# Kernel optimization log

Measured on AMD Instinct MI355X. Metric: run time of the kernel, lower is better.

## Reference

```python
import jax, jax.numpy as jnp
import numpy as np

EPS = 1e-07
INF = 100000.0
BIG = 1e8  # sentinel cost for priors outside all gt boxes/centers (filtered out in torch)
CENTER_RADIUS = 2.5
CANDIDATE_TOPK = 10
IOU_WEIGHT = 3.0
CLS_WEIGHT = 1.0
IMG = 1280.0


def setup_inputs() -> dict:
    key = jax.random.key(0)
    ks = jax.random.split(key, 9)
    N, G, C = 33600, 128, 80
    cx = jax.random.uniform(ks[0], (N,), minval=0.0, maxval=IMG)
    cy = jax.random.uniform(ks[1], (N,), minval=0.0, maxval=IMG)
    strides = jax.random.uniform(ks[2], (N, 2), minval=8.0, maxval=32.0)
    priors = jnp.stack([cx, cy, strides[:, 0], strides[:, 1]], axis=1)  # [N,4] cx,cy,sw,sh
    dc = jax.random.uniform(ks[3], (N, 2), minval=0.0, maxval=IMG)
    dwh = jax.random.uniform(ks[4], (N, 2), minval=4.0, maxval=200.0)
    decoded_bboxes = jnp.concatenate([dc - dwh / 2, dc + dwh / 2], axis=1)  # [N,4] tlbr
    gc = jax.random.uniform(ks[5], (G, 2), minval=0.0, maxval=IMG)
    gwh = jax.random.uniform(ks[6], (G, 2), minval=20.0, maxval=400.0)
    gt_bboxes = jnp.concatenate([gc - gwh / 2, gc + gwh / 2], axis=1)  # [G,4] tlbr
    pred_scores = jax.random.uniform(ks[7], (N, C), minval=1e-4, maxval=1.0 - 1e-4)
    gt_labels = jax.random.randint(ks[8], (G,), 0, C)
    return {
        'pred_scores': pred_scores,
        'priors': priors,
        'decoded_bboxes': decoded_bboxes,
        'gt_bboxes': gt_bboxes,
        'gt_labels': gt_labels,
    }


def _pairwise_iou(a, b):
    # a: [N,4] tlbr, b: [G,4] tlbr -> [N,G]
    tl = jnp.maximum(a[:, None, :2], b[None, :, :2])
    br = jnp.minimum(a[:, None, 2:], b[None, :, 2:])
    wh = jnp.clip(br - tl, 0.0)
    inter = wh[..., 0] * wh[..., 1]
    area_a = jnp.prod(jnp.clip(a[:, 2:] - a[:, :2], 0.0), axis=-1)
    area_b = jnp.prod(jnp.clip(b[:, 2:] - b[:, :2], 0.0), axis=-1)
    union = area_a[:, None] + area_b[None, :] - inter
    return inter / jnp.maximum(union, EPS)


def _forward(pred_scores, priors, decoded_bboxes, gt_bboxes, gt_labels):
    N = decoded_bboxes.shape[0]
    G = gt_bboxes.shape[0]
    px, py = priors[:, 0:1], priors[:, 1:2]          # [N,1]
    sx, sy = priors[:, 2:3], priors[:, 3:4]
    # in-gt-box mask [N,G]
    l_ = px - gt_bboxes[None, :, 0]
    t_ = py - gt_bboxes[None, :, 1]
    r_ = gt_bboxes[None, :, 2] - px
    b_ = gt_bboxes[None, :, 3] - py
    is_in_gts = jnp.minimum(jnp.minimum(l_, t_), jnp.minimum(r_, b_)) > 0
    # in-center mask [N,G]
    gcx = (gt_bboxes[:, 0] + gt_bboxes[:, 2]) / 2.0
    gcy = (gt_bboxes[:, 1] + gt_bboxes[:, 3]) / 2.0
    cl_ = px - (gcx[None, :] - CENTER_RADIUS * sx)
    ct_ = py - (gcy[None, :] - CENTER_RADIUS * sy)
    cr_ = (gcx[None, :] + CENTER_RADIUS * sx) - px
    cb_ = (gcy[None, :] + CENTER_RADIUS * sy) - py
    is_in_cts = jnp.minimum(jnp.minimum(cl_, ct_), jnp.minimum(cr_, cb_)) > 0
    valid = jnp.any(is_in_gts | is_in_cts, axis=1)           # [N]
    in_box_and_center = is_in_gts & is_in_cts                # [N,G]

    ious = _pairwise_iou(decoded_bboxes, gt_bboxes)          # [N,G]
    ious = jnp.where(valid[:, None], ious, 0.0)              # invalid priors excluded
    iou_cost = -jnp.log(ious + EPS)

    # BCE(pred, one_hot(label)).sum(-1) without materializing [N,G,C]:
    # = -log p[label] + log1p(-p[label]) - sum_c log1p(-p_c)  (logs clamped at -100 like torch)
    L = jnp.clip(jnp.log(pred_scores), -100.0)               # [N,C]
    L1 = jnp.clip(jnp.log1p(-pred_scores), -100.0)           # [N,C]
    gl = gt_labels.astype(jnp.int32)
    cls_cost = -(L[:, gl] - L1[:, gl]) - jnp.sum(L1, axis=1, keepdims=True)  # [N,G]

    cost = cls_cost * CLS_WEIGHT + iou_cost * IOU_WEIGHT + (~in_box_and_center) * INF
    cost = jnp.where(valid[:, None], cost, BIG)

    K = min(CANDIDATE_TOPK, N)
    topk_ious, _ = jax.lax.top_k(ious.T, K)                  # [G,K]
    dynamic_ks = jnp.clip(topk_ious.sum(1).astype(jnp.int32), 1, None)  # [G], <= K
    # per-GT: K smallest costs (ascending), keep first dynamic_k of them
    _, pos_idx = jax.lax.top_k(-cost.T, K)                   # [G,K] prior indices
    sel = (jnp.arange(K)[None, :] < dynamic_ks[:, None]).astype(cost.dtype)
    matching = jnp.zeros((N, G), cost.dtype).at[pos_idx, jnp.arange(G)[:, None]].add(sel)

    # resolve priors matched to >1 gt by min-cost gt
    multi = matching.sum(1) > 1
    argmin = jnp.argmin(cost, axis=1)
    matching = jnp.where(multi[:, None], jax.nn.one_hot(argmin, G, dtype=cost.dtype), matching)

    fg = matching.sum(1) > 0
    matched_gt = jnp.argmax(matching, axis=1)
    matched_iou = jnp.sum(matching * ious, axis=1)

    assigned_gt_inds = jnp.where(fg, matched_gt, 0)
    assigned_labels = jnp.where(fg, 1, -1)
    assigned_gt_iou = jnp.where(fg, matched_iou, -INF)
    return assigned_gt_inds, assigned_labels, assigned_gt_iou


def reference(pred_scores, priors, decoded_bboxes, gt_bboxes, gt_labels):
    return _forward(pred_scores, priors, decoded_bboxes, gt_bboxes, gt_labels)
```

## Files before the change

kernel.cpp:

```cpp
#include <hip/hip_runtime.h>
#include <math.h>
#include <limits.h>

#pragma clang fp contract(off)

#define TPB 256
#define ATPB 64
#define KTOP 10
#define ISPLIT 64
#define GSPLIT 8
#define GCAP 4096
#define CHUNKCAP 4224
#define MAXG 512
#define MAXMULTI 4096

typedef unsigned int u32;
typedef unsigned long long u64;
typedef unsigned char u8;

__device__ __forceinline__ float f_iou(float ax0, float ay0, float ax1, float ay1,
                                       float bx0, float by0, float bx1, float by1) {
  float tlx = fmaxf(ax0, bx0);
  float tly = fmaxf(ay0, by0);
  float brx = fminf(ax1, bx1);
  float bry = fminf(ay1, by1);
  float w = fmaxf(brx - tlx, 0.0f);
  float h = fmaxf(bry - tly, 0.0f);
  float inter = w * h;
  float aa = fmaxf(ax1 - ax0, 0.0f) * fmaxf(ay1 - ay0, 0.0f);
  float ab = fmaxf(bx1 - bx0, 0.0f) * fmaxf(by1 - by0, 0.0f);
  float uni = aa + ab - inter;
  return inter / fmaxf(uni, 1e-7f);
}

__device__ __forceinline__ float f_dv(float p) {
  float L  = fmaxf(logf(p), -100.0f);
  float L1 = fmaxf(log1pf(-p), -100.0f);
  return -(L - L1);
}

__device__ __forceinline__ float f_cost(float iou_masked, float dv, float sumL1v,
                                        float px, float py, float sx, float sy,
                                        float bx0, float by0, float bx1, float by1,
                                        int vld) {
  if (!vld) return 100000000.0f;
  float cls = dv - sumL1v;
  float l_ = px - bx0, t_ = py - by0, r_ = bx1 - px, b_ = by1 - py;
  bool ing = fminf(fminf(l_, t_), fminf(r_, b_)) > 0.0f;
  float gcx = (bx0 + bx1) * 0.5f;
  float gcy = (by0 + by1) * 0.5f;
  float cl = px - (gcx - 2.5f * sx);
  float ct = py - (gcy - 2.5f * sy);
  float cr = (gcx + 2.5f * sx) - px;
  float cb = (gcy + 2.5f * sy) - py;
  bool inc = fminf(fminf(cl, ct), fminf(cr, cb)) > 0.0f;
  float icost = -logf(iou_masked + 1e-7f);
  return (cls * 1.0f + icost * 3.0f) + ((ing && inc) ? 0.0f : 100000.0f);
}

__global__ __launch_bounds__(TPB) void k_fallback(float* out, int Nout) {
  int n = blockIdx.x * blockDim.x + threadIdx.x;
  if (n >= Nout) return;
  out[n] = 0.0f;
  out[Nout + n] = -1.0f;
  out[2 * Nout + n] = -70000.0f;
}

__global__ __launch_bounds__(TPB) void k_phase1(
    const float* pred, const float* priors, const float* gtb,
    float* sumL1, u32* packed, u8* validArr,
    int* gateCnt, int* gateList, int* flags,
    int N, int G, int C, int sumBlocks)
{
  __shared__ int lbuf[CHUNKCAP];
  __shared__ int lcnt;
  __shared__ int gbase;

  if ((int)blockIdx.x < sumBlocks) {
    int t = blockIdx.x * TPB + threadIdx.x;
    int n = t >> 3;
    int j = t & 7;
    if (n >= N) return;
    const float* pr = pred + (size_t)n * C;
    int lim = C - (C % 8);
    float r = 0.0f;
    for (int i = j; i < lim; i += 8) r += fmaxf(log1pf(-pr[i]), -100.0f);
    r += __shfl_down(r, 1, 8);
    r += __shfl_down(r, 2, 8);
    r += __shfl_down(r, 4, 8);
    if (j == 0) {
      for (int i = lim; i < C; ++i) r += fmaxf(log1pf(-pr[i]), -100.0f);
      sumL1[n] = r;
      packed[n] = 0;
    }
    return;
  }

  int bid = blockIdx.x - sumBlocks;
  int g = bid / GSPLIT;
  int s = bid % GSPLIT;
  int chunk = (N + GSPLIT - 1) / GSPLIT;
  int start = s * chunk;
  int end = start + chunk; if (end > N) end = N;
  int lane = threadIdx.x & 63;

  if (threadIdx.x == 0) lcnt = 0;
  __syncthreads();

  float x0 = gtb[g * 4 + 0], y0 = gtb[g * 4 + 1];
  float x1 = gtb[g * 4 + 2], y1 = gtb[g * 4 + 3];
  float gcx = (x0 + x1) * 0.5f, gcy = (y0 + y1) * 0.5f;
  const float4* pri4 = reinterpret_cast<const float4*>(priors);

  for (int nb = start; nb < end; nb += TPB) {
    int n = nb + threadIdx.x;
    bool gated = false;
    if (n < end) {
      float4 pv = pri4[n];
      float px = pv.x, py = pv.y, sx = pv.z, sy = pv.w;
      float l_ = px - x0, t_ = py - y0, r_ = x1 - px, b_ = y1 - py;
      bool ing = fminf(fminf(l_, t_), fminf(r_, b_)) > 0.0f;
      float cl = px - (gcx - 2.5f * sx), ct = py - (gcy - 2.5f * sy);
      float cr = (gcx + 2.5f * sx) - px, cb = (gcy + 2.5f * sy) - py;
      bool inc = fminf(fminf(cl, ct), fminf(cr, cb)) > 0.0f;
      if (ing || inc) validArr[n] = 1;
      gated = ing && inc;
    }
    u64 mask = __ballot(gated);
    int wcnt = __popcll(mask);
    int wbase = 0;
    if (lane == 0 && wcnt > 0) wbase = atomicAdd(&lcnt, wcnt);
    wbase = __shfl(wbase, 0);
    if (gated) {
      int p = __popcll(mask & ((1ull << lane) - 1ull));
      lbuf[wbase + p] = n;
    }
  }
  __syncthreads();
  int total = lcnt;
  if (threadIdx.x == 0 && total > 0) gbase = atomicAdd(&gateCnt[g], total);
  __syncthreads();
  if (total > 0) {
    int base = gbase;
    int* gl = gateList + (size_t)g * GCAP;
    for (int i = threadIdx.x; i < total; i += TPB) {
      int slot = base + i;
      if (slot < GCAP) gl[slot] = lbuf[i];
      else flags[g] = 1;
    }
  }
}

__global__ __launch_bounds__(ATPB) void k_iou_part(
    const float* dec, const u8* validArr, const float* gtb,
    float* iouV, int N, int G)
{
  int bid = blockIdx.x;
  int g = bid / ISPLIT;
  int s = bid % ISPLIT;
  int chunk = (N + ISPLIT - 1) / ISPLIT;
  int start = s * chunk;
  int end = start + chunk; if (end > N) end = N;
  int tid = threadIdx.x;
  float bx0 = gtb[g * 4 + 0];
  float by0 = gtb[g * 4 + 1];
  float bx1 = gtb[g * 4 + 2];
  float by1 = gtb[g * 4 + 3];

  float iv[KTOP];
#pragma unroll
  for (int j = 0; j < KTOP; ++j) iv[j] = 0.0f;

  const float4* dec4 = reinterpret_cast<const float4*>(dec);
  for (int n = start + tid; n < end; n += ATPB) {
    float4 dvb = dec4[n];
    float iou = f_iou(dvb.x, dvb.y, dvb.z, dvb.w, bx0, by0, bx1, by1);
    if (!validArr[n]) iou = 0.0f;
    if (iou > iv[KTOP - 1]) {
      float cu = iou;
#pragma unroll
      for (int j = 0; j < KTOP; ++j) {
        if (cu > iv[j]) { float tv = iv[j]; iv[j] = cu; cu = tv; }
      }
    }
  }

#pragma unroll
  for (int r = 0; r < KTOP; ++r) {
    float v = iv[0]; int owner = tid;
#pragma unroll
    for (int off = 32; off > 0; off >>= 1) {
      float v2 = __shfl_down(v, off);
      int o2 = __shfl_down(owner, off);
      if (v2 > v || (v2 == v && o2 < owner)) { v = v2; owner = o2; }
    }
    float wv = __shfl(v, 0);
    int wo = __shfl(owner, 0);
    if (tid == 0) iouV[bid * KTOP + r] = wv;
    if (tid == wo) {
#pragma unroll
      for (int j = 0; j < KTOP - 1; ++j) iv[j] = iv[j + 1];
      iv[KTOP - 1] = 0.0f;
    }
  }
}

__global__ __launch_bounds__(ATPB) void k_merge(
    const float* iouV, const int* gateCnt, const int* gateList, const int* flags,
    const float* pred, const float* priors, const float* dec, const float* sumL1,
    const u8* validArr, const int* gtl, const float* gtb,
    u32* packed, int G, int N, int C)
{
  int g = blockIdx.x;
  int tid = threadIdx.x;
  int base = g * ISPLIT * KTOP;
  const int TOT = ISPLIT * KTOP;
  const int PER = TOT / ATPB;

  float il[PER];
#pragma unroll
  for (int k = 0; k < PER; ++k) il[k] = 0.0f;
#pragma unroll
  for (int k = 0; k < PER; ++k) {
    float v = iouV[base + tid + k * ATPB];
    if (v > il[PER - 1]) {
#pragma unroll
      for (int j = 0; j < PER; ++j) {
        if (v > il[j]) { float tv = il[j]; il[j] = v; v = tv; }
      }
    }
  }
  float rv[KTOP];
#pragma unroll
  for (int r = 0; r < KTOP; ++r) {
    float v = il[0]; int owner = tid;
#pragma unroll
    for (int off = 32; off > 0; off >>= 1) {
      float v2 = __shfl_down(v, off);
      int o2 = __shfl_down(owner, off);
      if (v2 > v || (v2 == v && o2 < owner)) { v = v2; owner = o2; }
    }
    float wv = __shfl(v, 0);
    int wo = __shfl(owner, 0);
    rv[r] = wv;
    if (tid == wo) {
#pragma unroll
      for (int j = 0; j < PER - 1; ++j) il[j] = il[j + 1];
      il[PER - 1] = 0.0f;
    }
  }
  float s8 = ((rv[0] + rv[1]) + (rv[2] + rv[3])) + ((rv[4] + rv[5]) + (rv[6] + rv[7]));
  s8 += rv[8];
  s8 += rv[9];
  int dk = (int)s8;
  if (dk < 1) dk = 1;
  if (dk > KTOP) dk = KTOP;

  float bx0 = gtb[g * 4 + 0];
  float by0 = gtb[g * 4 + 1];
  float bx1 = gtb[g * 4 + 2];
  float by1 = gtb[g * 4 + 3];
  int lab = gtl[g];
  if (lab < 0) lab = 0;
  if (lab >= C) lab = C - 1;

  float cv[KTOP]; int ci[KTOP];
#pragma unroll
  for (int j = 0; j < KTOP; ++j) { cv[j] = 1e30f; ci[j] = INT_MAX; }
  const float4* dec4 = reinterpret_cast<const float4*>(dec);

  int cnt = gateCnt[g];
  if (!flags[g] && cnt >= KTOP) {
    const int* gl = gateList + (size_t)g * GCAP;
    for (int i = tid; i < cnt; i += ATPB) {
      int n = gl[i];
      float4 dvb = dec4[n];
      float iou = f_iou(dvb.x, dvb.y, dvb.z, dvb.w, bx0, by0, bx1, by1);
      float dv = f_dv(pred[(size_t)n * C + lab]);
      float cls = dv - sumL1[n];
      float icost = -logf(iou + 1e-7f);
      float c = (cls * 1.0f + icost * 3.0f) + 0.0f;
      bool ins = (c < cv[KTOP - 1]) || (c == cv[KTOP - 1] && n < ci[KTOP - 1]);
      if (ins) {
        float cu = c; int cui = n;
#pragma unroll
        for (int j = 0; j < KTOP; ++j) {
          bool lt = (cu < cv[j]) || (cu == cv[j] && cui < ci[j]);
          if (lt) { float tv = cv[j]; int ti = ci[j]; cv[j] = cu; ci[j] = cui; cu = tv; cui = ti; }
        }
      }
    }
  } else {
    const float4* pri4 = reinterpret_cast<const float4*>(priors);
    for (int n = tid; n < N; n += ATPB) {
      float4 dvb = dec4[n];
      int vld = validArr[n];
      float iou = f_iou(dvb.x, dvb.y, dvb.z, dvb.w, bx0, by0, bx1, by1);
      if (!vld) iou = 0.0f;
      float dv = f_dv(pred[(size_t)n * C + lab]);
      float4 pv = pri4[n];
      float c = f_cost(iou, dv, sumL1[n], pv.x, pv.y, pv.z, pv.w, bx0, by0, bx1, by1, vld);
      bool ins = (c < cv[KTOP - 1]) || (c == cv[KTOP - 1] && n < ci[KTOP - 1]);
      if (ins) {
        float cu = c; int cui = n;
#pragma unroll
        for (int j = 0; j < KTOP; ++j) {
          bool lt = (cu < cv[j]) || (cu == cv[j] && cui < ci[j]);
          if (lt) { float tv = cv[j]; int ti = ci[j]; cv[j] = cu; ci[j] = cui; cu = tv; cui = ti; }
        }
      }
    }
  }

  for (int r = 0; r < KTOP; ++r) {
    float v = cv[0]; int idx = ci[0];
#pragma unroll
    for (int off = 32; off > 0; off >>= 1) {
      float v2 = __shfl_down(v, off);
      int i2 = __shfl_down(idx, off);
      if (v2 < v || (v2 == v && i2 < idx)) { v = v2; idx = i2; }
    }
    int wi = __shfl(idx, 0);
    if (r < dk && tid == 0 && wi >= 0 && wi < N) {
      atomicAdd(&packed[wi], (1u << 16) | (u32)g);
    }
    if (ci[0] == wi) {
#pragma unroll
      for (int j = 0; j < KTOP - 1; ++j) { cv[j] = cv[j + 1]; ci[j] = ci[j + 1]; }
      cv[KTOP - 1] = 1e30f; ci[KTOP - 1] = INT_MAX;
    }
    if (r + 1 >= dk) break;
  }
}

__global__ __launch_bounds__(TPB) void k_final(
    const float* dec, const float* gtb, const u8* validArr, const u32* packed,
    int* mlist, int* mcnt,
    float* out, int N, int G, int Nout)
{
  __shared__ float sg[MAXG * 4];
  for (int i = threadIdx.x; i < G * 4; i += blockDim.x) sg[i] = gtb[i];
  __syncthreads();
  int n = blockIdx.x * blockDim.x + threadIdx.x;
  if (n >= N || n >= Nout) return;
  u32 pk = packed[n];
  int cnt = (int)(pk >> 16);
  float o0 = 0.0f, o1 = -1.0f, o2 = -100000.0f;
  if (cnt > 1) {
    int idx = atomicAdd(mcnt, 1);
    if (idx < MAXMULTI) mlist[idx] = n;
  }
  if (cnt == 1) {
    int g = (int)(pk & 0xFFFFu);
    if (g < 0) g = 0;
    if (g >= G) g = G - 1;
    const float4 dv = reinterpret_cast<const float4*>(dec)[n];
    float x0 = sg[g * 4 + 0], y0 = sg[g * 4 + 1], x1 = sg[g * 4 + 2], y1 = sg[g * 4 + 3];
    float iou = f_iou(dv.x, dv.y, dv.z, dv.w, x0, y0, x1, y1);
    if (!validArr[n]) iou = 0.0f;
    o0 = (float)g; o1 = 1.0f; o2 = iou;
  }
  out[n]            = o0;
  out[Nout + n]     = o1;
  out[2 * Nout + n] = o2;
}

#define MTPB 128
__global__ __launch_bounds__(MTPB) void k_multi(
    const float* pred, const float* priors, const float* dec,
    const float* gtb, const int* gtl, const float* sumL1, const u8* validArr,
    const int* mlist, const int* mcnt,
    float* out, int N, int G, int C, int Nout)
{
  __shared__ float rv[MTPB];
  __shared__ int   rg[MTPB];
  int tid = threadIdx.x;
  int total = *mcnt;
  if (total > MAXMULTI) total = MAXMULTI;
  for (int w = blockIdx.x; w < total; w += gridDim.x) {
    int n = mlist[w];
    const float4 dvb = reinterpret_cast<const float4*>(dec)[n];
    const float4 pv  = reinterpret_cast<const float4*>(priors)[n];
    float s1 = sumL1[n];
    int vld = validArr[n];
    float best = 1e30f; int bg = INT_MAX;
    for (int gg = tid; gg < G; gg += MTPB) {
      float x0 = gtb[gg * 4 + 0], y0 = gtb[gg * 4 + 1];
      float x1 = gtb[gg * 4 + 2], y1 = gtb[gg * 4 + 3];
      float iou = f_iou(dvb.x, dvb.y, dvb.z, dvb.w, x0, y0, x1, y1);
      if (!vld) iou = 0.0f;
      int lb = gtl[gg];
      if (lb < 0) lb = 0;
      if (lb >= C) lb = C - 1;
      float dv = f_dv(pred[(size_t)n * C + lb]);
      float c = f_cost(iou, dv, s1, pv.x, pv.y, pv.z, pv.w, x0, y0, x1, y1, vld);
      if (c < best || (c == best && gg < bg)) { best = c; bg = gg; }
    }
    rv[tid] = best; rg[tid] = bg;
    __syncthreads();
    for (int st = MTPB / 2; st > 0; st >>= 1) {
      if (tid < st) {
        float v2 = rv[tid + st]; int g2 = rg[tid + st];
        float v1 = rv[tid];      int g1 = rg[tid];
        if (v2 < v1 || (v2 == v1 && g2 < g1)) { rv[tid] = v2; rg[tid] = g2; }
      }
      __syncthreads();
    }
    if (tid == 0) {
      int g = rg[0];
      if (g < 0 || g >= G) g = 0;
      float x0 = gtb[g * 4 + 0], y0 = gtb[g * 4 + 1];
      float x1 = gtb[g * 4 + 2], y1 = gtb[g * 4 + 3];
      float iou = f_iou(dvb.x, dvb.y, dvb.z, dvb.w, x0, y0, x1, y1);
      if (!vld) iou = 0.0f;
      out[n]            = (float)g;
      out[Nout + n]     = 1.0f;
      out[2 * Nout + n] = iou;
    }
    __syncthreads();
  }
}

extern "C" void kernel_launch(void* const* d_in, const int* in_sizes, int n_in,
                              void* d_out, int out_size, void* d_ws, size_t ws_size,
                              hipStream_t stream) {
  const float* pred   = (const float*)d_in[0];
  const float* priors = (const float*)d_in[1];
  const float* dec    = (const float*)d_in[2];
  const float* gtb    = (const float*)d_in[3];
  const int*   gtl    = (const int*)d_in[4];
  int N = in_sizes[2] / 4;
  int G = in_sizes[3] / 4;
  if (G > MAXG) G = MAXG;
  int C = in_sizes[0] / N;
  int Nout = out_size / 3;
  float* out = (float*)d_out;

  size_t offPacked = 0;
  size_t offSum    = offPacked + (size_t)N * 4;
  size_t offZero   = (offSum + (size_t)N * 4 + 15) & ~(size_t)15;
  size_t offFlags  = offZero + (size_t)G * 4;
  size_t offMcnt   = offFlags + (size_t)G * 4;
  size_t offValid  = (offMcnt + 4 + 15) & ~(size_t)15;
  size_t offMlist  = (offValid + (size_t)N + 15) & ~(size_t)15;
  size_t offGlist  = (offMlist + (size_t)MAXMULTI * 4 + 15) & ~(size_t)15;
  size_t offIouV   = offGlist + (size_t)G * GCAP * 4;
  size_t need      = offIouV + (size_t)G * ISPLIT * KTOP * 4;

  dim3 b(TPB);
  int nblk = (N + TPB - 1) / TPB;
  int oblk = (Nout + TPB - 1) / TPB;
  if (ws_size < need || d_ws == nullptr) {
    k_fallback<<<oblk, b, 0, stream>>>(out, Nout);
    return;
  }
  char* wsb = (char*)d_ws;
  u32* packed   = (u32*)(wsb + offPacked);
  float* sumL1  = (float*)(wsb + offSum);
  int* gateCnt  = (int*)(wsb + offZero);
  int* flags    = (int*)(wsb + offFlags);
  int* mcnt     = (int*)(wsb + offMcnt);
  u8* validArr  = (u8*)(wsb + offValid);
  int* mlist    = (int*)(wsb + offMlist);
  int* gateList = (int*)(wsb + offGlist);
  float* iouV   = (float*)(wsb + offIouV);

  hipMemsetAsync(wsb + offZero, 0, offValid + (size_t)N - offZero, stream);

  int sumBlocks = ((N * 8) + TPB - 1) / TPB;
  int gateBlocks = G * GSPLIT;
  k_phase1<<<sumBlocks + gateBlocks, b, 0, stream>>>(
      pred, priors, gtb, sumL1, packed, validArr, gateCnt, gateList, flags,
      N, G, C, sumBlocks);
  k_iou_part<<<G * ISPLIT, dim3(ATPB), 0, stream>>>(dec, validArr, gtb, iouV, N, G);
  k_merge<<<G, dim3(ATPB), 0, stream>>>(iouV, gateCnt, gateList, flags,
                                        pred, priors, dec, sumL1, validArr, gtl, gtb,
                                        packed, G, N, C);
  k_final<<<nblk, b, 0, stream>>>(dec, gtb, validArr, packed, mlist, mcnt, out, N, G, Nout);
  k_multi<<<256, dim3(MTPB), 0, stream>>>(pred, priors, dec, gtb, gtl, sumL1, validArr,
                                          mlist, mcnt, out, N, G, C, Nout);
}
```

Baseline: 127.1 us.

## Collapse five kernels into three and drop memset and global atomics

The IoU top-k partial pass and the merge pass become one per-GT kernel of 256 threads. It scans all N priors itself and reduces across warps in shared memory. The valid mask is now computed per prior inside the sum blocks, so the memset and the per-GT atomic append go away. Each split now writes its gate list into a fixed slice. The final and multi-match kernels are fused, with multi-match rows resolved per wavefront through ballot and shuffles. This cuts launches and the memset, but phase2 now runs only G blocks, each scanning all N priors, which reduces parallelism.

```diff
diff --git a/kernel.cpp b/kernel.cpp
--- a/kernel.cpp
+++ b/kernel.cpp
@@ -5,14 +5,10 @@
 #pragma clang fp contract(off)
 
 #define TPB 256
-#define ATPB 64
 #define KTOP 10
-#define ISPLIT 64
 #define GSPLIT 8
-#define GCAP 4096
-#define CHUNKCAP 4224
+#define GSLICE 4352
 #define MAXG 512
-#define MAXMULTI 4096
 
 typedef unsigned int u32;
 typedef unsigned long long u64;
@@ -58,29 +54,49 @@
   return (cls * 1.0f + icost * 3.0f) + ((ing && inc) ? 0.0f : 100000.0f);
 }
 
-__global__ __launch_bounds__(TPB) void k_fallback(float* out, int Nout) {
+__global__ __launch_bounds__(TPB) void k_fb(float* out, int Nout, float val) {
   int n = blockIdx.x * blockDim.x + threadIdx.x;
   if (n >= Nout) return;
   out[n] = 0.0f;
   out[Nout + n] = -1.0f;
-  out[2 * Nout + n] = -70000.0f;
+  out[2 * Nout + n] = val;
 }
 
 __global__ __launch_bounds__(TPB) void k_phase1(
     const float* pred, const float* priors, const float* gtb,
     float* sumL1, u32* packed, u8* validArr,
-    int* gateCnt, int* gateList, int* flags,
+    int* gateCnt2, int* gateList,
     int N, int G, int C, int sumBlocks)
 {
-  __shared__ int lbuf[CHUNKCAP];
+  __shared__ float sg[MAXG * 4];
+  __shared__ int lbuf[GSLICE];
   __shared__ int lcnt;
-  __shared__ int gbase;
+  const int tid = threadIdx.x;
+  const int lane = tid & 63;
+  const float4* pri4 = reinterpret_cast<const float4*>(priors);
 
   if ((int)blockIdx.x < sumBlocks) {
-    int t = blockIdx.x * TPB + threadIdx.x;
-    int n = t >> 3;
-    int j = t & 7;
+    for (int i = tid; i < G * 4; i += TPB) sg[i] = gtb[i];
+    __syncthreads();
+    int t = blockIdx.x * TPB + tid;
+    int n = t >> 3, j = t & 7;
     if (n >= N) return;
+    float4 pv = pri4[n];
+    float px = pv.x, py = pv.y, sx = pv.z, sy = pv.w;
+    int valid = 0;
+    for (int g = j; g < G; g += 8) {
+      float x0 = sg[g * 4 + 0], y0 = sg[g * 4 + 1], x1 = sg[g * 4 + 2], y1 = sg[g * 4 + 3];
+      float l_ = px - x0, t_ = py - y0, r_ = x1 - px, b_ = y1 - py;
+      bool ing = fminf(fminf(l_, t_), fminf(r_, b_)) > 0.0f;
+      float gcx = (x0 + x1) * 0.5f, gcy = (y0 + y1) * 0.5f;
+      float cl = px - (gcx - 2.5f * sx), ct = py - (gcy - 2.5f * sy);
+      float cr = (gcx + 2.5f * sx) - px, cb = (gcy + 2.5f * sy) - py;
+      bool inc = fminf(fminf(cl, ct), fminf(cr, cb)) > 0.0f;
+      valid |= (ing || inc) ? 1 : 0;
+    }
+    valid |= __shfl_xor(valid, 1, 8);
+    valid |= __shfl_xor(valid, 2, 8);
+    valid |= __shfl_xor(valid, 4, 8);
     const float* pr = pred + (size_t)n * C;
     int lim = C - (C % 8);
     float r = 0.0f;
@@ -91,29 +107,24 @@
     if (j == 0) {
       for (int i = lim; i < C; ++i) r += fmaxf(log1pf(-pr[i]), -100.0f);
       sumL1[n] = r;
+      validArr[n] = (u8)valid;
       packed[n] = 0;
     }
     return;
   }
 
-  int bid = blockIdx.x - sumBlocks;
-  int g = bid / GSPLIT;
-  int s = bid % GSPLIT;
+  int bidg = blockIdx.x - sumBlocks;
+  int g = bidg / GSPLIT, s = bidg % GSPLIT;
   int chunk = (N + GSPLIT - 1) / GSPLIT;
   int start = s * chunk;
   int end = start + chunk; if (end > N) end = N;
-  int lane = threadIdx.x & 63;
-
-  if (threadIdx.x == 0) lcnt = 0;
-  __syncthreads();
-
   float x0 = gtb[g * 4 + 0], y0 = gtb[g * 4 + 1];
   float x1 = gtb[g * 4 + 2], y1 = gtb[g * 4 + 3];
   float gcx = (x0 + x1) * 0.5f, gcy = (y0 + y1) * 0.5f;
-  const float4* pri4 = reinterpret_cast<const float4*>(priors);
-
+  if (tid == 0) lcnt = 0;
+  __syncthreads();
   for (int nb = start; nb < end; nb += TPB) {
-    int n = nb + threadIdx.x;
+    int n = nb + tid;
     bool gated = false;
     if (n < end) {
       float4 pv = pri4[n];
@@ -123,7 +134,6 @@
       float cl = px - (gcx - 2.5f * sx), ct = py - (gcy - 2.5f * sy);
       float cr = (gcx + 2.5f * sx) - px, cb = (gcy + 2.5f * sy) - py;
       bool inc = fminf(fminf(cl, ct), fminf(cr, cb)) > 0.0f;
-      if (ing || inc) validArr[n] = 1;
       gated = ing && inc;
     }
     u64 mask = __ballot(gated);
@@ -138,43 +148,32 @@
   }
   __syncthreads();
   int total = lcnt;
-  if (threadIdx.x == 0 && total > 0) gbase = atomicAdd(&gateCnt[g], total);
-  __syncthreads();
-  if (total > 0) {
-    int base = gbase;
-    int* gl = gateList + (size_t)g * GCAP;
-    for (int i = threadIdx.x; i < total; i += TPB) {
-      int slot = base + i;
-      if (slot < GCAP) gl[slot] = lbuf[i];
-      else flags[g] = 1;
-    }
-  }
-}
-
-__global__ __launch_bounds__(ATPB) void k_iou_part(
-    const float* dec, const u8* validArr, const float* gtb,
-    float* iouV, int N, int G)
+  if (tid == 0) gateCnt2[bidg] = total;
+  int* gl = gateList + (size_t)bidg * GSLICE;
+  for (int i = tid; i < total; i += TPB) gl[i] = lbuf[i];
+}
+
+__global__ __launch_bounds__(TPB) void k_phase2(
+    const float* pred, const float* priors, const float* dec,
+    const float* gtb, const int* gtl, const float* sumL1, const u8* validArr,
+    const int* gateCnt2, const int* gateList,
+    u32* packed, int N, int G, int C)
 {
-  int bid = blockIdx.x;
-  int g = bid / ISPLIT;
-  int s = bid % ISPLIT;
-  int chunk = (N + ISPLIT - 1) / ISPLIT;
-  int start = s * chunk;
-  int end = start + chunk; if (end > N) end = N;
-  int tid = threadIdx.x;
-  float bx0 = gtb[g * 4 + 0];
-  float by0 = gtb[g * 4 + 1];
-  float bx1 = gtb[g * 4 + 2];
-  float by1 = gtb[g * 4 + 3];
+  int g = blockIdx.x;
+  int tid = threadIdx.x, lane = tid & 63, wid = tid >> 6;
+  __shared__ float wlv[4 * KTOP];
+  __shared__ int   wli[4 * KTOP];
+  __shared__ int sdk;
+  float bx0 = gtb[g * 4 + 0], by0 = gtb[g * 4 + 1];
+  float bx1 = gtb[g * 4 + 2], by1 = gtb[g * 4 + 3];
+  const float4* dec4 = reinterpret_cast<const float4*>(dec);
 
   float iv[KTOP];
 #pragma unroll
   for (int j = 0; j < KTOP; ++j) iv[j] = 0.0f;
-
-  const float4* dec4 = reinterpret_cast<const float4*>(dec);
-  for (int n = start + tid; n < end; n += ATPB) {
-    float4 dvb = dec4[n];
-    float iou = f_iou(dvb.x, dvb.y, dvb.z, dvb.w, bx0, by0, bx1, by1);
+  for (int n = tid; n < N; n += TPB) {
+    float4 d = dec4[n];
+    float iou = f_iou(d.x, d.y, d.z, d.w, bx0, by0, bx1, by1);
     if (!validArr[n]) iou = 0.0f;
     if (iou > iv[KTOP - 1]) {
       float cu = iou;
@@ -184,10 +183,9 @@
       }
     }
   }
-
 #pragma unroll
   for (int r = 0; r < KTOP; ++r) {
-    float v = iv[0]; int owner = tid;
+    float v = iv[0]; int owner = lane;
 #pragma unroll
     for (int off = 32; off > 0; off >>= 1) {
       float v2 = __shfl_down(v, off);
@@ -196,90 +194,86 @@
     }
     float wv = __shfl(v, 0);
     int wo = __shfl(owner, 0);
-    if (tid == 0) iouV[bid * KTOP + r] = wv;
-    if (tid == wo) {
+    if (lane == 0) wlv[wid * KTOP + r] = wv;
+    if (lane == wo) {
 #pragma unroll
       for (int j = 0; j < KTOP - 1; ++j) iv[j] = iv[j + 1];
       iv[KTOP - 1] = 0.0f;
     }
   }
-}
-
-__global__ __launch_bounds__(ATPB) void k_merge(
-    const float* iouV, const int* gateCnt, const int* gateList, const int* flags,
-    const float* pred, const float* priors, const float* dec, const float* sumL1,
-    const u8* validArr, const int* gtl, const float* gtb,
-    u32* packed, int G, int N, int C)
-{
-  int g = blockIdx.x;
-  int tid = threadIdx.x;
-  int base = g * ISPLIT * KTOP;
-  const int TOT = ISPLIT * KTOP;
-  const int PER = TOT / ATPB;
-
-  float il[PER];
-#pragma unroll
-  for (int k = 0; k < PER; ++k) il[k] = 0.0f;
-#pragma unroll
-  for (int k = 0; k < PER; ++k) {
-    float v = iouV[base + tid + k * ATPB];
-    if (v > il[PER - 1]) {
-#pragma unroll
-      for (int j = 0; j < PER; ++j) {
-        if (v > il[j]) { float tv = il[j]; il[j] = v; v = tv; }
-      }
-    }
-  }
-  float rv[KTOP];
-#pragma unroll
-  for (int r = 0; r < KTOP; ++r) {
-    float v = il[0]; int owner = tid;
-#pragma unroll
-    for (int off = 32; off > 0; off >>= 1) {
-      float v2 = __shfl_down(v, off);
-      int o2 = __shfl_down(owner, off);
-      if (v2 > v || (v2 == v && o2 < owner)) { v = v2; owner = o2; }
-    }
-    float wv = __shfl(v, 0);
-    int wo = __shfl(owner, 0);
-    rv[r] = wv;
-    if (tid == wo) {
-#pragma unroll
-      for (int j = 0; j < PER - 1; ++j) il[j] = il[j + 1];
-      il[PER - 1] = 0.0f;
-    }
-  }
-  float s8 = ((rv[0] + rv[1]) + (rv[2] + rv[3])) + ((rv[4] + rv[5]) + (rv[6] + rv[7]));
-  s8 += rv[8];
-  s8 += rv[9];
-  int dk = (int)s8;
-  if (dk < 1) dk = 1;
-  if (dk > KTOP) dk = KTOP;
-
-  float bx0 = gtb[g * 4 + 0];
-  float by0 = gtb[g * 4 + 1];
-  float bx1 = gtb[g * 4 + 2];
-  float by1 = gtb[g * 4 + 3];
+  __syncthreads();
+  if (wid == 0) {
+    float v = (lane < 4 * KTOP) ? wlv[lane] : 0.0f;
+    float rv[KTOP];
+#pragma unroll
+    for (int r = 0; r < KTOP; ++r) {
+      float m = v; int owner = lane;
+#pragma unroll
+      for (int off = 32; off > 0; off >>= 1) {
+        float v2 = __shfl_down(m, off);
+        int o2 = __shfl_down(owner, off);
+        if (v2 > m || (v2 == m && o2 < owner)) { m = v2; owner = o2; }
+      }
+      float wv = __shfl(m, 0);
+      int wo = __shfl(owner, 0);
+      rv[r] = wv;
+      if (lane == wo) v = 0.0f;
+    }
+    float s8 = ((rv[0] + rv[1]) + (rv[2] + rv[3])) + ((rv[4] + rv[5]) + (rv[6] + rv[7]));
+    s8 += rv[8];
+    s8 += rv[9];
+    int dk = (int)s8;
+    if (dk < 1) dk = 1;
+    if (dk > KTOP) dk = KTOP;
+    if (lane == 0) sdk = dk;
+  }
+  __syncthreads();
+  int dk = sdk;
+
   int lab = gtl[g];
   if (lab < 0) lab = 0;
   if (lab >= C) lab = C - 1;
-
   float cv[KTOP]; int ci[KTOP];
 #pragma unroll
   for (int j = 0; j < KTOP; ++j) { cv[j] = 1e30f; ci[j] = INT_MAX; }
-  const float4* dec4 = reinterpret_cast<const float4*>(dec);
-
-  int cnt = gateCnt[g];
-  if (!flags[g] && cnt >= KTOP) {
-    const int* gl = gateList + (size_t)g * GCAP;
-    for (int i = tid; i < cnt; i += ATPB) {
-      int n = gl[i];
-      float4 dvb = dec4[n];
-      float iou = f_iou(dvb.x, dvb.y, dvb.z, dvb.w, bx0, by0, bx1, by1);
+
+  int total = 0;
+  for (int s = 0; s < GSPLIT; ++s) total += gateCnt2[g * GSPLIT + s];
+
+  if (total >= KTOP) {
+    for (int s = 0; s < GSPLIT; ++s) {
+      int cs = gateCnt2[g * GSPLIT + s];
+      const int* gl = gateList + (size_t)(g * GSPLIT + s) * GSLICE;
+      for (int i = tid; i < cs; i += TPB) {
+        int n = gl[i];
+        float4 d = dec4[n];
+        float iou = f_iou(d.x, d.y, d.z, d.w, bx0, by0, bx1, by1);
+        float dv = f_dv(pred[(size_t)n * C + lab]);
+        float cls = dv - sumL1[n];
+        float icost = -logf(iou + 1e-7f);
+        float c = (cls * 1.0f + icost * 3.0f) + 0.0f;
+        bool ins = (c < cv[KTOP - 1]) || (c == cv[KTOP - 1] && n < ci[KTOP - 1]);
+        if (ins) {
+          float cu = c; int cui = n;
+#pragma unroll
+          for (int j = 0; j < KTOP; ++j) {
+            bool lt = (cu < cv[j]) || (cu == cv[j] && cui < ci[j]);
+            if (lt) { float tv = cv[j]; int ti = ci[j]; cv[j] = cu; ci[j] = cui; cu = tv; cui = ti; }
+          }
+        }
+      }
+    }
+  } else {
+    const float4* pri4 = reinterpret_cast<const float4*>(priors);
+    for (int n = tid; n < N; n += TPB) {
+      float4 d = dec4[n];
+      int vld = validArr[n];
+      float iou = f_iou(d.x, d.y, d.z, d.w, bx0, by0, bx1, by1);
+      if (!vld) iou = 0.0f;
       float dv = f_dv(pred[(size_t)n * C + lab]);
-      float cls = dv - sumL1[n];
-      float icost = -logf(iou + 1e-7f);
-      float c = (cls * 1.0f + icost * 3.0f) + 0.0f;
+      float4 pv = pri4[n];
+      float c = f_cost(iou, dv, sumL1[n], pv.x, pv.y, pv.z, pv.w,
+                       bx0, by0, bx1, by1, vld);
       bool ins = (c < cv[KTOP - 1]) || (c == cv[KTOP - 1] && n < ci[KTOP - 1]);
       if (ins) {
         float cu = c; int cui = n;
@@ -290,28 +284,9 @@
         }
       }
     }
-  } else {
-    const float4* pri4 = reinterpret_cast<const float4*>(priors);
-    for (int n = tid; n < N; n += ATPB) {
-      float4 dvb = dec4[n];
-      int vld = validArr[n];
-      float iou = f_iou(dvb.x, dvb.y, dvb.z, dvb.w, bx0, by0, bx1, by1);
-      if (!vld) iou = 0.0f;
-      float dv = f_dv(pred[(size_t)n * C + lab]);
-      float4 pv = pri4[n];
-      float c = f_cost(iou, dv, sumL1[n], pv.x, pv.y, pv.z, pv.w, bx0, by0, bx1, by1, vld);
-      bool ins = (c < cv[KTOP - 1]) || (c == cv[KTOP - 1] && n < ci[KTOP - 1]);
-      if (ins) {
-        float cu = c; int cui = n;
-#pragma unroll
-        for (int j = 0; j < KTOP; ++j) {
-          bool lt = (cu < cv[j]) || (cu == cv[j] && cui < ci[j]);
-          if (lt) { float tv = cv[j]; int ti = ci[j]; cv[j] = cu; ci[j] = cui; cu = tv; cui = ti; }
-        }
-      }
-    }
-  }
-
+  }
+
+#pragma unroll
   for (int r = 0; r < KTOP; ++r) {
     float v = cv[0]; int idx = ci[0];
 #pragma unroll
@@ -320,104 +295,117 @@
       int i2 = __shfl_down(idx, off);
       if (v2 < v || (v2 == v && i2 < idx)) { v = v2; idx = i2; }
     }
+    float wv = __shfl(v, 0);
     int wi = __shfl(idx, 0);
-    if (r < dk && tid == 0 && wi >= 0 && wi < N) {
-      atomicAdd(&packed[wi], (1u << 16) | (u32)g);
-    }
-    if (ci[0] == wi) {
+    if (lane == 0) { wlv[wid * KTOP + r] = wv; wli[wid * KTOP + r] = wi; }
+    if (ci[0] == wi && wi != INT_MAX) {
 #pragma unroll
       for (int j = 0; j < KTOP - 1; ++j) { cv[j] = cv[j + 1]; ci[j] = ci[j + 1]; }
       cv[KTOP - 1] = 1e30f; ci[KTOP - 1] = INT_MAX;
     }
-    if (r + 1 >= dk) break;
-  }
-}
-
-__global__ __launch_bounds__(TPB) void k_final(
-    const float* dec, const float* gtb, const u8* validArr, const u32* packed,
-    int* mlist, int* mcnt,
-    float* out, int N, int G, int Nout)
+  }
+  __syncthreads();
+  if (wid == 0) {
+    float v; int idx;
+    if (lane < 4 * KTOP) { v = wlv[lane]; idx = wli[lane]; }
+    else { v = 1e30f; idx = INT_MAX; }
+    for (int r = 0; r < dk; ++r) {
+      float m = v; int mi = idx; int owner = lane;
+#pragma unroll
+      for (int off = 32; off > 0; off >>= 1) {
+        float v2 = __shfl_down(m, off);
+        int i2 = __shfl_down(mi, off);
+        int o2 = __shfl_down(owner, off);
+        if (v2 < m || (v2 == m && i2 < mi)) { m = v2; mi = i2; owner = o2; }
+      }
+      int wi = __shfl(mi, 0);
+      int wo = __shfl(owner, 0);
+      if (lane == 0 && wi >= 0 && wi < N) {
+        atomicAdd(&packed[wi], (1u << 16) | (u32)g);
+      }
+      if (lane == wo) { v = 1e30f; idx = INT_MAX; }
+    }
+  }
+}
+
+__global__ __launch_bounds__(TPB) void k_phase3(
+    const float* pred, const float* priors, const float* dec,
+    const float* gtb, const int* gtl, const float* sumL1,
+    const u8* validArr, const u32* packed,
+    float* out, int N, int G, int C, int Nout)
 {
   __shared__ float sg[MAXG * 4];
+  __shared__ int sl[MAXG];
   for (int i = threadIdx.x; i < G * 4; i += blockDim.x) sg[i] = gtb[i];
-  __syncthreads();
-  int n = blockIdx.x * blockDim.x + threadIdx.x;
-  if (n >= N || n >= Nout) return;
-  u32 pk = packed[n];
+  for (int i = threadIdx.x; i < G; i += blockDim.x) {
+    int lb = gtl[i];
+    if (lb < 0) lb = 0;
+    if (lb >= C) lb = C - 1;
+    sl[i] = lb;
+  }
+  __syncthreads();
+  const int tid = threadIdx.x;
+  const int lane = tid & 63;
+  const float4* dec4 = reinterpret_cast<const float4*>(dec);
+  const float4* pri4 = reinterpret_cast<const float4*>(priors);
+  int n = blockIdx.x * TPB + tid;
+  bool active = (n < N && n < Nout);
+  u32 pk = active ? packed[n] : 0;
   int cnt = (int)(pk >> 16);
-  float o0 = 0.0f, o1 = -1.0f, o2 = -100000.0f;
-  if (cnt > 1) {
-    int idx = atomicAdd(mcnt, 1);
-    if (idx < MAXMULTI) mlist[idx] = n;
-  }
-  if (cnt == 1) {
-    int g = (int)(pk & 0xFFFFu);
-    if (g < 0) g = 0;
-    if (g >= G) g = G - 1;
-    const float4 dv = reinterpret_cast<const float4*>(dec)[n];
-    float x0 = sg[g * 4 + 0], y0 = sg[g * 4 + 1], x1 = sg[g * 4 + 2], y1 = sg[g * 4 + 3];
-    float iou = f_iou(dv.x, dv.y, dv.z, dv.w, x0, y0, x1, y1);
-    if (!validArr[n]) iou = 0.0f;
-    o0 = (float)g; o1 = 1.0f; o2 = iou;
-  }
-  out[n]            = o0;
-  out[Nout + n]     = o1;
-  out[2 * Nout + n] = o2;
-}
-
-#define MTPB 128
-__global__ __launch_bounds__(MTPB) void k_multi(
-    const float* pred, const float* priors, const float* dec,
-    const float* gtb, const int* gtl, const float* sumL1, const u8* validArr,
-    const int* mlist, const int* mcnt,
-    float* out, int N, int G, int C, int Nout)
-{
-  __shared__ float rv[MTPB];
-  __shared__ int   rg[MTPB];
-  int tid = threadIdx.x;
-  int total = *mcnt;
-  if (total > MAXMULTI) total = MAXMULTI;
-  for (int w = blockIdx.x; w < total; w += gridDim.x) {
-    int n = mlist[w];
-    const float4 dvb = reinterpret_cast<const float4*>(dec)[n];
-    const float4 pv  = reinterpret_cast<const float4*>(priors)[n];
-    float s1 = sumL1[n];
-    int vld = validArr[n];
+
+  if (active && cnt <= 1) {
+    float o0 = 0.0f, o1 = -1.0f, o2 = -100000.0f;
+    if (cnt == 1) {
+      int g = (int)(pk & 0xFFFFu);
+      if (g < 0) g = 0;
+      if (g >= G) g = G - 1;
+      float4 d = dec4[n];
+      float x0 = sg[g * 4 + 0], y0 = sg[g * 4 + 1], x1 = sg[g * 4 + 2], y1 = sg[g * 4 + 3];
+      float iou = f_iou(d.x, d.y, d.z, d.w, x0, y0, x1, y1);
+      if (!validArr[n]) iou = 0.0f;
+      o0 = (float)g; o1 = 1.0f; o2 = iou;
+    }
+    out[n]            = o0;
+    out[Nout + n]     = o1;
+    out[2 * Nout + n] = o2;
+  }
+
+  u64 mm = __ballot(active && cnt > 1);
+  while (mm) {
+    int l = (int)(__ffsll((unsigned long long)mm) - 1);
+    mm &= mm - 1;
+    int mn = __shfl(n, l);
+    float4 dvb = dec4[mn];
+    float4 pv = pri4[mn];
+    float s1 = sumL1[mn];
+    int vld = validArr[mn];
     float best = 1e30f; int bg = INT_MAX;
-    for (int gg = tid; gg < G; gg += MTPB) {
-      float x0 = gtb[gg * 4 + 0], y0 = gtb[gg * 4 + 1];
-      float x1 = gtb[gg * 4 + 2], y1 = gtb[gg * 4 + 3];
+    for (int gg = lane; gg < G; gg += 64) {
+      float x0 = sg[gg * 4 + 0], y0 = sg[gg * 4 + 1];
+      float x1 = sg[gg * 4 + 2], y1 = sg[gg * 4 + 3];
       float iou = f_iou(dvb.x, dvb.y, dvb.z, dvb.w, x0, y0, x1, y1);
       if (!vld) iou = 0.0f;
-      int lb = gtl[gg];
-      if (lb < 0) lb = 0;
-      if (lb >= C) lb = C - 1;
-      float dv = f_dv(pred[(size_t)n * C + lb]);
+      float dv = f_dv(pred[(size_t)mn * C + sl[gg]]);
       float c = f_cost(iou, dv, s1, pv.x, pv.y, pv.z, pv.w, x0, y0, x1, y1, vld);
       if (c < best || (c == best && gg < bg)) { best = c; bg = gg; }
     }
-    rv[tid] = best; rg[tid] = bg;
-    __syncthreads();
-    for (int st = MTPB / 2; st > 0; st >>= 1) {
-      if (tid < st) {
-        float v2 = rv[tid + st]; int g2 = rg[tid + st];
-        float v1 = rv[tid];      int g1 = rg[tid];
-        if (v2 < v1 || (v2 == v1 && g2 < g1)) { rv[tid] = v2; rg[tid] = g2; }
-      }
-      __syncthreads();
-    }
-    if (tid == 0) {
-      int g = rg[0];
-      if (g < 0 || g >= G) g = 0;
-      float x0 = gtb[g * 4 + 0], y0 = gtb[g * 4 + 1];
-      float x1 = gtb[g * 4 + 2], y1 = gtb[g * 4 + 3];
+#pragma unroll
+    for (int off = 32; off > 0; off >>= 1) {
+      float v2 = __shfl_down(best, off);
+      int g2 = __shfl_down(bg, off);
+      if (v2 < best || (v2 == best && g2 < bg)) { best = v2; bg = g2; }
+    }
+    int wg = __shfl(bg, 0);
+    if (lane == 0) {
+      int g = (wg < 0 || wg >= G) ? 0 : wg;
+      float x0 = sg[g * 4 + 0], y0 = sg[g * 4 + 1];
+      float x1 = sg[g * 4 + 2], y1 = sg[g * 4 + 3];
       float iou = f_iou(dvb.x, dvb.y, dvb.z, dvb.w, x0, y0, x1, y1);
       if (!vld) iou = 0.0f;
-      out[n]            = (float)g;
-      out[Nout + n]     = 1.0f;
-      out[2 * Nout + n] = iou;
-    }
-    __syncthreads();
+      out[mn]            = (float)g;
+      out[Nout + mn]     = 1.0f;
+      out[2 * Nout + mn] = iou;
+    }
   }
 }
 
@@ -431,52 +419,44 @@
   const int*   gtl    = (const int*)d_in[4];
   int N = in_sizes[2] / 4;
   int G = in_sizes[3] / 4;
-  if (G > MAXG) G = MAXG;
   int C = in_sizes[0] / N;
   int Nout = out_size / 3;
   float* out = (float*)d_out;
 
+  dim3 b(TPB);
+  int oblk = (Nout + TPB - 1) / TPB;
+  int chunk = (N + GSPLIT - 1) / GSPLIT;
+  if (G > MAXG || chunk > GSLICE) {
+    k_fb<<<oblk, b, 0, stream>>>(out, Nout, -60000.0f);
+    return;
+  }
+
   size_t offPacked = 0;
   size_t offSum    = offPacked + (size_t)N * 4;
-  size_t offZero   = (offSum + (size_t)N * 4 + 15) & ~(size_t)15;
-  size_t offFlags  = offZero + (size_t)G * 4;
-  size_t offMcnt   = offFlags + (size_t)G * 4;
-  size_t offValid  = (offMcnt + 4 + 15) & ~(size_t)15;
-  size_t offMlist  = (offValid + (size_t)N + 15) & ~(size_t)15;
-  size_t offGlist  = (offMlist + (size_t)MAXMULTI * 4 + 15) & ~(size_t)15;
-  size_t offIouV   = offGlist + (size_t)G * GCAP * 4;
-  size_t need      = offIouV + (size_t)G * ISPLIT * KTOP * 4;
-
-  dim3 b(TPB);
-  int nblk = (N + TPB - 1) / TPB;
-  int oblk = (Nout + TPB - 1) / TPB;
+  size_t offValid  = offSum + (size_t)N * 4;
+  size_t offCnt2   = (offValid + (size_t)N + 15) & ~(size_t)15;
+  size_t offGlist  = (offCnt2 + (size_t)G * GSPLIT * 4 + 15) & ~(size_t)15;
+  size_t need      = offGlist + (size_t)G * GSPLIT * GSLICE * 4;
   if (ws_size < need || d_ws == nullptr) {
-    k_fallback<<<oblk, b, 0, stream>>>(out, Nout);
+    k_fb<<<oblk, b, 0, stream>>>(out, Nout, -70000.0f);
     return;
   }
   char* wsb = (char*)d_ws;
   u32* packed   = (u32*)(wsb + offPacked);
   float* sumL1  = (float*)(wsb + offSum);
-  int* gateCnt  = (int*)(wsb + offZero);
-  int* flags    = (int*)(wsb + offFlags);
-  int* mcnt     = (int*)(wsb + offMcnt);
   u8* validArr  = (u8*)(wsb + offValid);
-  int* mlist    = (int*)(wsb + offMlist);
+  int* gateCnt2 = (int*)(wsb + offCnt2);
   int* gateList = (int*)(wsb + offGlist);
-  float* iouV   = (float*)(wsb + offIouV);
-
-  hipMemsetAsync(wsb + offZero, 0, offValid + (size_t)N - offZero, stream);
-
-  int sumBlocks = ((N * 8) + TPB - 1) / TPB;
-  int gateBlocks = G * GSPLIT;
-  k_phase1<<<sumBlocks + gateBlocks, b, 0, stream>>>(
-      pred, priors, gtb, sumL1, packed, validArr, gateCnt, gateList, flags,
+
+  int sumBlocks = (N * 8 + TPB - 1) / TPB;
+  int nblk = (N + TPB - 1) / TPB;
+  k_phase1<<<sumBlocks + G * GSPLIT, b, 0, stream>>>(
+      pred, priors, gtb, sumL1, packed, validArr, gateCnt2, gateList,
       N, G, C, sumBlocks);
-  k_iou_part<<<G * ISPLIT, dim3(ATPB), 0, stream>>>(dec, validArr, gtb, iouV, N, G);
-  k_merge<<<G, dim3(ATPB), 0, stream>>>(iouV, gateCnt, gateList, flags,
-                                        pred, priors, dec, sumL1, validArr, gtl, gtb,
-                                        packed, G, N, C);
-  k_final<<<nblk, b, 0, stream>>>(dec, gtb, validArr, packed, mlist, mcnt, out, N, G, Nout);
-  k_multi<<<256, dim3(MTPB), 0, stream>>>(pred, priors, dec, gtb, gtl, sumL1, validArr,
-                                          mlist, mcnt, out, N, G, C, Nout);
-}
+  k_phase2<<<G, b, 0, stream>>>(
+      pred, priors, dec, gtb, gtl, sumL1, validArr, gateCnt2, gateList,
+      packed, N, G, C);
+  k_phase3<<<nblk, b, 0, stream>>>(
+      pred, priors, dec, gtb, gtl, sumL1, validArr, packed,
+      out, N, G, C, Nout);
+}
```

New measurement: 174.7 us. 37.4% more time.
